# Performance work log

Measured on AMD Instinct MI355X. Metric: run time of the kernel, lower is better.

Reference implementation:

```python
import jax, jax.numpy as jnp
import numpy as np

D_MODEL = 1024
NHEAD = 16
HEAD_DIM = D_MODEL // NHEAD
ROPE_BASE = 10000.0


def rotate_half(x):
    h = x.shape[-1] // 2
    return jnp.concatenate((-x[..., h:], x[..., :h]), axis=-1)


def rope_cos_sin(seq_len, dim, dtype):
    inv_freq = 1.0 / (ROPE_BASE ** (jnp.arange(0, dim, 2, dtype=jnp.float32) / dim))
    t = jnp.arange(seq_len, dtype=jnp.float32)
    freqs = jnp.einsum('i,j->ij', t, inv_freq)  # [S, dim/2]
    emb = jnp.concatenate((freqs, freqs), axis=-1)  # [S, dim]
    return jnp.cos(emb).astype(dtype), jnp.sin(emb).astype(dtype)


def setup_inputs() -> dict:
    key = jax.random.key(0)
    ks = jax.random.split(key, 9)
    b, s = 2, 2048
    lim = 1.0 / np.sqrt(D_MODEL)
    def lin(kw, kb):
        W = jax.random.uniform(kw, (D_MODEL, D_MODEL), jnp.float32, -lim, lim)
        bia = jax.random.uniform(kb, (D_MODEL,), jnp.float32, -lim, lim)
        return W, bia
    Wq, bq = lin(ks[0], ks[1])
    Wk, bk = lin(ks[2], ks[3])
    Wv, bv = lin(ks[4], ks[5])
    Wo, bo = lin(ks[6], ks[7])
    x = jax.random.normal(ks[8], (b, s, D_MODEL), jnp.float32)
    return {"x": x, "Wq": Wq, "bq": bq, "Wk": Wk, "bk": bk,
            "Wv": Wv, "bv": bv, "Wo": Wo, "bo": bo}


def reference(x, Wq, bq, Wk, bk, Wv, bv, Wo, bo):
    b, s, _ = x.shape
    scale = jnp.sqrt(jnp.asarray(HEAD_DIM, x.dtype))
    # projections (torch Linear: y = x @ W.T + b)
    q = x @ Wq.T + bq
    k = x @ Wk.T + bk
    v = x @ Wv.T + bv
    # [b, h, s, d]
    def split_heads(t):
        return t.reshape(b, s, NHEAD, HEAD_DIM).transpose(0, 2, 1, 3)
    q, k, v = split_heads(q), split_heads(k), split_heads(v)
    cos, sin = rope_cos_sin(s, HEAD_DIM, x.dtype)  # [s, d]
    q = q * cos + rotate_half(q) * sin
    k = k * cos + rotate_half(k) * sin
    scores = jnp.einsum('bhqd,bhkd->bhqk', q, k) / scale
    probs = jax.nn.softmax(scores, axis=-1)
    out = jnp.einsum('bhqk,bhkd->bhqd', probs, v)
    out = out.transpose(0, 2, 1, 3).reshape(b, s, D_MODEL)
    return out @ Wo.T + bo
```

## Files before the change

kernel.cpp:

```cpp
#include <hip/hip_runtime.h>
#include <hip/hip_bf16.h>
#include <stdint.h>


typedef __attribute__((ext_vector_type(8))) short bf16x8;
typedef __attribute__((ext_vector_type(4))) float f32x4;
typedef __attribute__((ext_vector_type(16))) float f32x16;
typedef __attribute__((ext_vector_type(4))) short short4v;
typedef __attribute__((ext_vector_type(4))) float float4v;
typedef __attribute__((ext_vector_type(4))) unsigned uint32x4;

#define DEV __device__ __forceinline__

DEV short f2bf(float f) {
  union { float f; uint32_t u; } v; v.f = f;
  uint32_t r = (v.u + 0x7fffu + ((v.u >> 16) & 1u)) >> 16;
  return (short)(uint16_t)r;
}
DEV float bf2f(short b) {
  union { uint32_t u; float f; } v; v.u = ((uint32_t)(uint16_t)b) << 16;
  return v.f;
}
DEV unsigned cvtpk(float a, float b) {
  unsigned d;
  asm("v_cvt_pk_bf16_f32 %0, %1, %2" : "=v"(d) : "v"(a), "v"(b));
  return d;
}
DEV void gload16(const void* g, const void* l) {
  __builtin_amdgcn_global_load_lds((const __attribute__((address_space(1))) void*)g,
                                   (__attribute__((address_space(3))) void*)l, 16, 0, 0);
}

__global__ void convert_kernel(const float* __restrict__ x,
                               const float* __restrict__ wq, const float* __restrict__ wk,
                               const float* __restrict__ wv, const float* __restrict__ wo,
                               short* __restrict__ xb, short* __restrict__ wqb,
                               short* __restrict__ wkb, short* __restrict__ wvb,
                               short* __restrict__ wob,
                               float* __restrict__ ct, float* __restrict__ st) {
  const int idx = blockIdx.x * blockDim.x + threadIdx.x;
  if (idx >= 2097152) {
    const int i2 = idx - 2097152;
    const int t = i2 >> 5, j = i2 & 31;
    const float f = (float)t * exp2f(-(float)j * (13.287712379549449f / 32.f));
    ct[i2] = cosf(f);
    st[i2] = sinf(f);
    return;
  }
  const float* src; short* dst; int off;
  if (idx < 1048576)      { src = x;  dst = xb;  off = idx; }
  else if (idx < 1310720) { src = wq; dst = wqb; off = idx - 1048576; }
  else if (idx < 1572864) { src = wk; dst = wkb; off = idx - 1310720; }
  else if (idx < 1835008) { src = wv; dst = wvb; off = idx - 1572864; }
  else                    { src = wo; dst = wob; off = idx - 1835008; }
  float4v v = *(const float4v*)(src + (size_t)off * 4);
  short4v o;
  o[0] = f2bf(v[0]); o[1] = f2bf(v[1]); o[2] = f2bf(v[2]); o[3] = f2bf(v[3]);
  *(short4v*)(dst + (size_t)off * 4) = o;
}

template<bool FINAL>
__global__ __launch_bounds__(256, 2) void gemm_bt(
    const short* __restrict__ A,
    const short* __restrict__ W0, const short* __restrict__ W1, const short* __restrict__ W2,
    const float* __restrict__ b0, const float* __restrict__ b1, const float* __restrict__ b2,
    short* __restrict__ o0, short* __restrict__ o1, short* __restrict__ o2,
    float* __restrict__ of,
    const float* __restrict__ ct, const float* __restrict__ st) {
  constexpr int K = 1024;
  __shared__ short lds[2 * 128 * 64];
  short* As = lds;
  short* Ws = lds + 128 * 64;

  const int tid = threadIdx.x;
  const int lane = tid & 63;
  const int w = tid >> 6;
  const int wr = w >> 1, wc = w & 1;
  const int bn = blockIdx.x, bm = blockIdx.y, z = blockIdx.z;

  const short* Wt = (z == 0) ? W0 : (z == 1 ? W1 : W2);
  const float* bias = (z == 0) ? b0 : (z == 1 ? b1 : b2);
  short* ob = (z == 0) ? o0 : (z == 1 ? o1 : o2);

  const int lrow = lane >> 3;
  const int clog = 16 * ((lane & 7) ^ lrow);

  f32x4 acc[4][4] = {};
  const size_t arowbase = (size_t)(bm * 128) * K;
  const size_t wrowbase = (size_t)(bn * 128) * K;

  for (int kt = 0; kt < K / 64; ++kt) {
    __syncthreads();
#pragma unroll
    for (int i = 0; i < 4; ++i) {
      const int c = i * 4 + w;
      const int row = c * 8 + lrow;
      gload16(A + arowbase + (size_t)row * K + kt * 64 + (clog >> 1),
              (const char*)As + c * 1024);
      gload16(Wt + wrowbase + (size_t)row * K + kt * 64 + (clog >> 1),
              (const char*)Ws + c * 1024);
    }
    __syncthreads();
#pragma unroll
    for (int kk = 0; kk < 2; ++kk) {
      bf16x8 af[4], bf[4];
      const int kb = (kk * 32 + (lane >> 4) * 8) * 2;
#pragma unroll
      for (int mi = 0; mi < 4; ++mi) {
        const int row = wr * 64 + mi * 16 + (lane & 15);
        af[mi] = *(const bf16x8*)((const char*)As + row * 128 + (kb ^ ((row & 7) << 4)));
      }
#pragma unroll
      for (int ni = 0; ni < 4; ++ni) {
        const int row = wc * 64 + ni * 16 + (lane & 15);
        bf[ni] = *(const bf16x8*)((const char*)Ws + row * 128 + (kb ^ ((row & 7) << 4)));
      }
#pragma unroll
      for (int mi = 0; mi < 4; ++mi)
#pragma unroll
        for (int ni = 0; ni < 4; ++ni)
          acc[mi][ni] = __builtin_amdgcn_mfma_f32_16x16x32_bf16(af[mi], bf[ni], acc[mi][ni], 0, 0, 0);
    }
  }

  float bv[4];
#pragma unroll
  for (int ni = 0; ni < 4; ++ni)
    bv[ni] = bias[bn * 128 + wc * 64 + ni * 16 + (lane & 15)];

#pragma unroll
  for (int mi = 0; mi < 4; ++mi) {
#pragma unroll
    for (int r = 0; r < 4; ++r) {
      const int m = bm * 128 + wr * 64 + mi * 16 + (lane >> 4) * 4 + r;
      float v[4];
#pragma unroll
      for (int ni = 0; ni < 4; ++ni) v[ni] = acc[mi][ni][r] + bv[ni];
      if (!FINAL && z < 2) {
        const int s = m & 2047;
        const float sc = (z == 0) ? 0.18033688011f : 1.0f;
#pragma unroll
        for (int jj = 0; jj < 2; ++jj) {
          const int j = jj * 16 + (lane & 15);
          const float c = ct[s * 32 + j] * sc, sn = st[s * 32 + j] * sc;
          const float a = v[jj], bb = v[jj + 2];
          v[jj]     = a * c - bb * sn;
          v[jj + 2] = bb * c + a * sn;
        }
      }
#pragma unroll
      for (int ni = 0; ni < 4; ++ni) {
        const int n = bn * 128 + wc * 64 + ni * 16 + (lane & 15);
        if (FINAL) {
          of[(size_t)m * 1024 + n] = v[ni];
        } else {
          const int b = m >> 11, s = m & 2047, h = n >> 6, d = n & 63;
          const int bh = b * 16 + h;
          if (z == 1) {
            const size_t fi =
                ((((((size_t)bh * 32 + (s >> 6)) * 2 + ((s >> 5) & 1)) * 4 + (d >> 4)) * 64
                  + ((s & 31) + ((d >> 3) & 1) * 32)) * 8) + (d & 7);
            ob[fi] = f2bf(v[ni]);
          } else {
            ob[(((size_t)bh) * 2048 + s) * 64 + d] = f2bf(v[ni]);
          }
        }
      }
    }
  }
}

__global__ void vtrans_kernel(const short* __restrict__ v, short* __restrict__ vt) {
  __shared__ short t[64][72];
  const int bh = blockIdx.x, st0 = blockIdx.y * 64;
  const int tid = threadIdx.x;
#pragma unroll
  for (int i = 0; i < 2; ++i) {
    const int j = i * 256 + tid;
    const int row = j >> 3, c8 = (j & 7) * 8;
    *(bf16x8*)&t[row][c8] = *(const bf16x8*)(v + (((size_t)bh * 2048) + st0 + row) * 64 + c8);
  }
  __syncthreads();
#pragma unroll
  for (int i = 0; i < 2; ++i) {
    const int j = i * 256 + tid;
    const int dd = j >> 3, s8 = (j & 7) * 8;
    const int b16 = s8 & ~15;
    const int hi8 = (s8 >> 3) & 1;
    bf16x8 o;
#pragma unroll
    for (int e = 0; e < 8; ++e)
      o[e] = t[b16 + 4 * hi8 + (e & 3) + 8 * (e >> 2)][dd];
    const int kv0 = st0 + s8;
    const int jg = kv0 >> 6, ts = (kv0 >> 4) & 3;
    const int db = dd >> 5, ln = (dd & 31) + 32 * hi8;
    *(bf16x8*)(vt + ((((size_t)bh * 32 + jg) * 4 + ts) * 2 + db) * 512 + ln * 8) = o;
  }
}

__global__ __launch_bounds__(256, 2) void attn_kernel(
    const short* __restrict__ q, const short* __restrict__ kfb,
    const short* __restrict__ vfb, short* __restrict__ ao) {
  __shared__ float fm[4 * 2112];

  const int tid = threadIdx.x, lane = tid & 63, w = tid >> 6;
  const int wg = w & 1, g = w >> 1;
  const int hi = lane >> 5;
  const int bh = blockIdx.x, qt = blockIdx.y;

  const int qrow0 = qt * 128 + wg * 64 + (lane & 31);
  const short* qb = q + ((size_t)bh * 2048 + qrow0) * 64 + hi * 8;
  bf16x8 qf0[4], qf1[4];
#pragma unroll
  for (int m = 0; m < 4; ++m) {
    qf0[m] = *(const bf16x8*)(qb + 16 * m);
    qf1[m] = *(const bf16x8*)(qb + 32 * 64 + 16 * m);
  }

  f32x16 acc0[2] = {}, acc1[2] = {};
  float l0 = 0.f, l1 = 0.f;

  const short* kp = kfb + (((size_t)bh * 32 + g * 16) * 8) * 512 + (size_t)lane * 8;
  const short* vp = vfb + (((size_t)bh * 32 + g * 16) * 8) * 512 + (size_t)lane * 8;

  bf16x8 kf[2][4];
#pragma unroll
  for (int t = 0; t < 2; ++t)
#pragma unroll
    for (int m = 0; m < 4; ++m)
      kf[t][m] = *(const bf16x8*)(kp + (t * 4 + m) * 512);
  kp += 4096;

  for (int j = 0; j < 16; ++j) {
    f32x16 stv0[2] = {}, stv1[2] = {};
#pragma unroll
    for (int t = 0; t < 2; ++t)
#pragma unroll
      for (int m = 0; m < 4; ++m) {
        stv0[t] = __builtin_amdgcn_mfma_f32_32x32x16_bf16(kf[t][m], qf0[m], stv0[t], 0, 0, 0);
        stv1[t] = __builtin_amdgcn_mfma_f32_32x32x16_bf16(kf[t][m], qf1[m], stv1[t], 0, 0, 0);
      }

    bf16x8 vv[2][2][2];
#pragma unroll
    for (int t = 0; t < 2; ++t)
#pragma unroll
      for (int sl = 0; sl < 2; ++sl)
#pragma unroll
        for (int db = 0; db < 2; ++db)
          vv[t][sl][db] = *(const bf16x8*)(vp + ((t * 2 + sl) * 2 + db) * 512);
    vp += 4096;
    if (j < 15) {
#pragma unroll
      for (int t = 0; t < 2; ++t)
#pragma unroll
        for (int m = 0; m < 4; ++m)
          kf[t][m] = *(const bf16x8*)(kp + (t * 4 + m) * 512);
      kp += 4096;
    }

#pragma unroll
    for (int t = 0; t < 2; ++t) {
#pragma unroll
      for (int r = 0; r < 16; ++r) {
        const float p0 = __builtin_amdgcn_exp2f(stv0[t][r]);
        const float p1 = __builtin_amdgcn_exp2f(stv1[t][r]);
        stv0[t][r] = p0; l0 += p0;
        stv1[t][r] = p1; l1 += p1;
      }
      uint32x4 pu0[2], pu1[2];
#pragma unroll
      for (int sl = 0; sl < 2; ++sl)
#pragma unroll
        for (int jj = 0; jj < 4; ++jj) {
          pu0[sl][jj] = cvtpk(stv0[t][8 * sl + 2 * jj], stv0[t][8 * sl + 2 * jj + 1]);
          pu1[sl][jj] = cvtpk(stv1[t][8 * sl + 2 * jj], stv1[t][8 * sl + 2 * jj + 1]);
        }
#pragma unroll
      for (int sl = 0; sl < 2; ++sl) {
        const bf16x8 pv0 = __builtin_bit_cast(bf16x8, pu0[sl]);
        const bf16x8 pv1 = __builtin_bit_cast(bf16x8, pu1[sl]);
#pragma unroll
        for (int db = 0; db < 2; ++db) {
          acc0[db] = __builtin_amdgcn_mfma_f32_32x32x16_bf16(vv[t][sl][db], pv0, acc0[db], 0, 0, 0);
          acc1[db] = __builtin_amdgcn_mfma_f32_32x32x16_bf16(vv[t][sl][db], pv1, acc1[db], 0, 0, 0);
        }
      }
    }
  }

  l0 += __shfl_xor(l0, 32);
  l1 += __shfl_xor(l1, 32);

  float* fm0 = fm + (wg * 2 + 0) * 2112;
  float* fm1 = fm + (wg * 2 + 1) * 2112;
  if (g == 1) {
    fm0[lane] = l0;
    fm1[lane] = l1;
#pragma unroll
    for (int db = 0; db < 2; ++db)
#pragma unroll
      for (int r = 0; r < 16; ++r) {
        fm0[64 + (db * 16 + r) * 64 + lane] = acc0[db][r];
        fm1[64 + (db * 16 + r) * 64 + lane] = acc1[db][r];
      }
  }
  __syncthreads();

  if (g == 0) {
    const int b = bh >> 4, h = bh & 15;
#pragma unroll
    for (int s = 0; s < 2; ++s) {
      float* fmp = s ? fm1 : fm0;
      f32x16* accp = s ? acc1 : acc0;
      const float rl = 1.0f / ((s ? l1 : l0) + fmp[lane]);
      const int qrow = qrow0 + 32 * s;
      short* orow = ao + ((size_t)b * 2048 + qrow) * 1024 + h * 64;
#pragma unroll
      for (int db = 0; db < 2; ++db)
#pragma unroll
        for (int gq = 0; gq < 4; ++gq) {
          short4v o;
#pragma unroll
          for (int jj = 0; jj < 4; ++jj) {
            const int r = 4 * gq + jj;
            const float v1 = fmp[64 + (db * 16 + r) * 64 + lane];
            o[jj] = f2bf((accp[db][r] + v1) * rl);
          }
          *(short4v*)(orow + db * 32 + 8 * gq + 4 * hi) = o;
        }
    }
  }
}

extern "C" void kernel_launch(void* const* d_in, const int* in_sizes, int n_in,
                              void* d_out, int out_size, void* d_ws, size_t ws_size,
                              hipStream_t stream) {
  const float* x  = (const float*)d_in[0];
  const float* Wq = (const float*)d_in[1];
  const float* bq = (const float*)d_in[2];
  const float* Wk = (const float*)d_in[3];
  const float* bk = (const float*)d_in[4];
  const float* Wv = (const float*)d_in[5];
  const float* bv = (const float*)d_in[6];
  const float* Wo = (const float*)d_in[7];
  const float* bo = (const float*)d_in[8];
  float* out = (float*)d_out;

  char* ws = (char*)d_ws;
  short* xb  = (short*)(ws);
  short* wqb = (short*)(ws + 8388608);
  short* wkb = (short*)(ws + 10485760);
  short* wvb = (short*)(ws + 12582912);
  short* wob = (short*)(ws + 14680064);
  float* ct  = (float*)(ws + 16777216);
  float* st  = (float*)(ws + 17039360);
  short* qb  = (short*)(ws + 17301504);
  short* kfb = (short*)(ws + 25690112);
  short* vb  = (short*)(ws + 34078720);
  short* vfb = (short*)(ws + 42467328);
  short* ab  = (short*)(ws + 50855936);

  convert_kernel<<<dim3(8448), dim3(256), 0, stream>>>(
      x, Wq, Wk, Wv, Wo, xb, wqb, wkb, wvb, wob, ct, st);
  gemm_bt<false><<<dim3(8, 32, 3), dim3(256), 0, stream>>>(
      xb, wqb, wkb, wvb, bq, bk, bv, qb, kfb, vb, (float*)nullptr, ct, st);
  vtrans_kernel<<<dim3(32, 32), dim3(256), 0, stream>>>(vb, vfb);
  attn_kernel<<<dim3(32, 16), dim3(256), 0, stream>>>(qb, kfb, vfb, ab);
  gemm_bt<true><<<dim3(8, 32, 1), dim3(256), 0, stream>>>(
      ab, wob, (short*)nullptr, (short*)nullptr, bo, (float*)nullptr, (float*)nullptr,
      (short*)nullptr, (short*)nullptr, (short*)nullptr, out, ct, st);
}
```

Before: 105.9 us.

## Fuse V transpose into QKV GEMM epilogue and split attention KV four ways

The QKV GEMM epilogue now writes V directly in the fragment-ordered layout the attention kernel consumes, which removes the separate vtrans kernel and its extra pass over V. The attention kernel also changes its work split: each block handles 64 query rows, and its four waves each take a quarter of the KV sequence. Partial sums are reduced serially through shared memory with extra barriers. The grid doubles to 32x32 blocks, giving more parallelism at the cost of more Q/K/V reloading and a longer reduction tail. The epilogue's V writes are now scattered 2-byte stores.

```diff
diff --git a/kernel.cpp b/kernel.cpp
--- a/kernel.cpp
+++ b/kernel.cpp
@@ -161,6 +161,14 @@
                 ((((((size_t)bh * 32 + (s >> 6)) * 2 + ((s >> 5) & 1)) * 4 + (d >> 4)) * 64
                   + ((s & 31) + ((d >> 3) & 1) * 32)) * 8) + (d & 7);
             ob[fi] = f2bf(v[ni]);
+          } else if (z == 2) {
+            const int rr = s & 15;
+            const int hi8 = (rr >> 2) & 1;
+            const int e = (rr & 3) + 4 * ((rr >> 3) & 1);
+            const size_t fi =
+                ((((size_t)bh * 32 + (s >> 6)) * 4 + ((s >> 4) & 3)) * 2 + (d >> 5)) * 512
+                + (size_t)((d & 31) + 32 * hi8) * 8 + e;
+            ob[fi] = f2bf(v[ni]);
           } else {
             ob[(((size_t)bh) * 2048 + s) * 64 + d] = f2bf(v[ni]);
           }
@@ -170,45 +178,16 @@
   }
 }
 
-__global__ void vtrans_kernel(const short* __restrict__ v, short* __restrict__ vt) {
-  __shared__ short t[64][72];
-  const int bh = blockIdx.x, st0 = blockIdx.y * 64;
-  const int tid = threadIdx.x;
-#pragma unroll
-  for (int i = 0; i < 2; ++i) {
-    const int j = i * 256 + tid;
-    const int row = j >> 3, c8 = (j & 7) * 8;
-    *(bf16x8*)&t[row][c8] = *(const bf16x8*)(v + (((size_t)bh * 2048) + st0 + row) * 64 + c8);
-  }
-  __syncthreads();
-#pragma unroll
-  for (int i = 0; i < 2; ++i) {
-    const int j = i * 256 + tid;
-    const int dd = j >> 3, s8 = (j & 7) * 8;
-    const int b16 = s8 & ~15;
-    const int hi8 = (s8 >> 3) & 1;
-    bf16x8 o;
-#pragma unroll
-    for (int e = 0; e < 8; ++e)
-      o[e] = t[b16 + 4 * hi8 + (e & 3) + 8 * (e >> 2)][dd];
-    const int kv0 = st0 + s8;
-    const int jg = kv0 >> 6, ts = (kv0 >> 4) & 3;
-    const int db = dd >> 5, ln = (dd & 31) + 32 * hi8;
-    *(bf16x8*)(vt + ((((size_t)bh * 32 + jg) * 4 + ts) * 2 + db) * 512 + ln * 8) = o;
-  }
-}
-
 __global__ __launch_bounds__(256, 2) void attn_kernel(
     const short* __restrict__ q, const short* __restrict__ kfb,
     const short* __restrict__ vfb, short* __restrict__ ao) {
-  __shared__ float fm[4 * 2112];
+  __shared__ float fm[2 * 2112];
 
   const int tid = threadIdx.x, lane = tid & 63, w = tid >> 6;
-  const int wg = w & 1, g = w >> 1;
   const int hi = lane >> 5;
   const int bh = blockIdx.x, qt = blockIdx.y;
 
-  const int qrow0 = qt * 128 + wg * 64 + (lane & 31);
+  const int qrow0 = qt * 64 + (lane & 31);
   const short* qb = q + ((size_t)bh * 2048 + qrow0) * 64 + hi * 8;
   bf16x8 qf0[4], qf1[4];
 #pragma unroll
@@ -220,8 +199,8 @@
   f32x16 acc0[2] = {}, acc1[2] = {};
   float l0 = 0.f, l1 = 0.f;
 
-  const short* kp = kfb + (((size_t)bh * 32 + g * 16) * 8) * 512 + (size_t)lane * 8;
-  const short* vp = vfb + (((size_t)bh * 32 + g * 16) * 8) * 512 + (size_t)lane * 8;
+  const short* kp = kfb + (((size_t)bh * 32 + w * 8) * 8) * 512 + (size_t)lane * 8;
+  const short* vp = vfb + (((size_t)bh * 32 + w * 8) * 8) * 512 + (size_t)lane * 8;
 
   bf16x8 kf[2][4];
 #pragma unroll
@@ -231,7 +210,7 @@
       kf[t][m] = *(const bf16x8*)(kp + (t * 4 + m) * 512);
   kp += 4096;
 
-  for (int j = 0; j < 16; ++j) {
+  for (int j = 0; j < 8; ++j) {
     f32x16 stv0[2] = {}, stv1[2] = {};
 #pragma unroll
     for (int t = 0; t < 2; ++t)
@@ -250,7 +229,7 @@
         for (int db = 0; db < 2; ++db)
           vv[t][sl][db] = *(const bf16x8*)(vp + ((t * 2 + sl) * 2 + db) * 512);
     vp += 4096;
-    if (j < 15) {
+    if (j < 7) {
 #pragma unroll
       for (int t = 0; t < 2; ++t)
 #pragma unroll
@@ -292,26 +271,46 @@
   l0 += __shfl_xor(l0, 32);
   l1 += __shfl_xor(l1, 32);
 
-  float* fm0 = fm + (wg * 2 + 0) * 2112;
-  float* fm1 = fm + (wg * 2 + 1) * 2112;
-  if (g == 1) {
-    fm0[lane] = l0;
-    fm1[lane] = l1;
+  float* f0 = fm;
+  float* f1 = fm + 2112;
+  if (w == 0) {
+    f0[lane] = l0; f1[lane] = l1;
 #pragma unroll
     for (int db = 0; db < 2; ++db)
 #pragma unroll
       for (int r = 0; r < 16; ++r) {
-        fm0[64 + (db * 16 + r) * 64 + lane] = acc0[db][r];
-        fm1[64 + (db * 16 + r) * 64 + lane] = acc1[db][r];
+        f0[64 + (db * 16 + r) * 64 + lane] = acc0[db][r];
+        f1[64 + (db * 16 + r) * 64 + lane] = acc1[db][r];
       }
   }
   __syncthreads();
-
-  if (g == 0) {
+  if (w == 1) {
+    f0[lane] += l0; f1[lane] += l1;
+#pragma unroll
+    for (int db = 0; db < 2; ++db)
+#pragma unroll
+      for (int r = 0; r < 16; ++r) {
+        f0[64 + (db * 16 + r) * 64 + lane] += acc0[db][r];
+        f1[64 + (db * 16 + r) * 64 + lane] += acc1[db][r];
+      }
+  }
+  __syncthreads();
+  if (w == 2) {
+    f0[lane] += l0; f1[lane] += l1;
+#pragma unroll
+    for (int db = 0; db < 2; ++db)
+#pragma unroll
+      for (int r = 0; r < 16; ++r) {
+        f0[64 + (db * 16 + r) * 64 + lane] += acc0[db][r];
+        f1[64 + (db * 16 + r) * 64 + lane] += acc1[db][r];
+      }
+  }
+  __syncthreads();
+  if (w == 3) {
     const int b = bh >> 4, h = bh & 15;
 #pragma unroll
     for (int s = 0; s < 2; ++s) {
-      float* fmp = s ? fm1 : fm0;
+      float* fmp = s ? f1 : f0;
       f32x16* accp = s ? acc1 : acc0;
       const float rl = 1.0f / ((s ? l1 : l0) + fmp[lane]);
       const int qrow = qrow0 + 32 * s;
@@ -357,16 +356,14 @@
   float* st  = (float*)(ws + 17039360);
   short* qb  = (short*)(ws + 17301504);
   short* kfb = (short*)(ws + 25690112);
-  short* vb  = (short*)(ws + 34078720);
   short* vfb = (short*)(ws + 42467328);
   short* ab  = (short*)(ws + 50855936);
 
   convert_kernel<<<dim3(8448), dim3(256), 0, stream>>>(
       x, Wq, Wk, Wv, Wo, xb, wqb, wkb, wvb, wob, ct, st);
   gemm_bt<false><<<dim3(8, 32, 3), dim3(256), 0, stream>>>(
-      xb, wqb, wkb, wvb, bq, bk, bv, qb, kfb, vb, (float*)nullptr, ct, st);
-  vtrans_kernel<<<dim3(32, 32), dim3(256), 0, stream>>>(vb, vfb);
-  attn_kernel<<<dim3(32, 16), dim3(256), 0, stream>>>(qb, kfb, vfb, ab);
+      xb, wqb, wkb, wvb, bq, bk, bv, qb, kfb, vfb, (float*)nullptr, ct, st);
+  attn_kernel<<<dim3(32, 32), dim3(256), 0, stream>>>(qb, kfb, vfb, ab);
   gemm_bt<true><<<dim3(8, 32, 1), dim3(256), 0, stream>>>(
       ab, wob, (short*)nullptr, (short*)nullptr, bo, (float*)nullptr, (float*)nullptr,
       (short*)nullptr, (short*)nullptr, (short*)nullptr, out, ct, st);
```

Result: no change. 107.0 us (+1.0%).
